# Performance work log

Hardware: AMD Instinct MI355X
Metric: run time of the kernel (lower is better)

Reference implementation:

```python
import jax, jax.numpy as jnp
from jax import lax
import numpy as np

N_NODES = 8192
N_FEATURES = 1024
N_FILTRATIONS = 4
HIDDEN_DIM = 64
MAX_DEG = 8            # fixed out-degree used when generating edge_list
N_EDGES = N_NODES * MAX_DEG


def setup_inputs() -> dict:
    key = jax.random.key(0)
    ks = jax.random.split(key, 10)
    X = jax.random.normal(ks[0], (N_NODES, N_FEATURES), dtype=jnp.float32)
    # directed edge list, exactly MAX_DEG out-edges per node
    src = jnp.repeat(jnp.arange(N_NODES, dtype=jnp.int32), MAX_DEG)
    dst = jax.random.randint(ks[1], (N_EDGES,), 0, N_NODES, dtype=jnp.int32)
    edge_list = jnp.stack([src, dst], axis=0)
    # filtrations_nn: Linear(n_features,32) -> ReLU -> Linear(32,n_filtrations)
    W1 = jax.random.normal(ks[2], (32, N_FEATURES), dtype=jnp.float32) * 0.05
    b1 = jnp.zeros((32,), jnp.float32)
    W2 = jax.random.normal(ks[3], (N_FILTRATIONS, 32), dtype=jnp.float32) * 0.05
    b2 = jnp.zeros((N_FILTRATIONS,), jnp.float32)
    # deep sets: theta = Linear(2*n_filtrations, hidden), rho = Linear(1, n_features)
    Wt = jax.random.normal(ks[4], (HIDDEN_DIM, 2 * N_FILTRATIONS), dtype=jnp.float32) * 0.05
    bt = jnp.zeros((HIDDEN_DIM,), jnp.float32)
    Wr = jax.random.normal(ks[5], (N_FEATURES, 1), dtype=jnp.float32) * 0.05
    br = jnp.zeros((N_FEATURES,), jnp.float32)
    return {"X": X, "edge_list": edge_list, "W1": W1, "b1": b1, "W2": W2,
            "b2": b2, "Wt": Wt, "bt": bt, "Wr": Wr, "br": br}


def uf_find(parent, node):
    # chase parent pointers until a root (parent[v] == v)
    return lax.while_loop(lambda v: parent[v] != v, lambda v: parent[v], node)


def build_neighbor_table(edge_list, n_nodes, max_deg):
    # padded CSR-style neighbor table (n_nodes, max_deg), -1 = no edge
    src = edge_list[0].astype(jnp.int32)
    dst = edge_list[1].astype(jnp.int32)
    e = src.shape[0]
    order_e = jnp.argsort(src)  # stable
    src_s, dst_s = src[order_e], dst[order_e]
    counts = jnp.zeros(n_nodes, jnp.int32).at[src].add(1)
    offsets = jnp.concatenate([jnp.zeros(1, jnp.int32), jnp.cumsum(counts)[:-1].astype(jnp.int32)])
    slot = jnp.arange(e, dtype=jnp.int32) - offsets[src_s]
    return jnp.full((n_nodes, max_deg), -1, jnp.int32).at[src_s, slot].set(dst_s)


def persistence_dim0(values, nbr_table):
    """0-dim persistence via sequential union-find with elder rule.
    Row for sort-position j: (birth=j, death=step when the component born at j is absorbed).
    Returned indexed by node id (diagram[order[j]] = row j), matching the torch code."""
    n = values.shape[0]
    order = jnp.argsort(values).astype(jnp.int32)  # filtration order
    pos = jnp.zeros(n, jnp.int32).at[order].set(jnp.arange(n, dtype=jnp.int32))  # rank
    parent0 = jnp.arange(n, dtype=jnp.int32)
    deaths0 = jnp.zeros(n, jnp.float32)

    def step_fn(carry, sv):
        parent, deaths = carry
        s, vertex = sv
        nbrs = nbr_table[vertex]

        def edge_body(k, pc):
            parent, deaths = pc
            u = nbrs[k]
            u_c = jnp.maximum(u, 0)
            valid = (u >= 0) & (pos[u_c] <= s)  # neighbor already activated
            u_eff = jnp.where(valid, u_c, vertex)
            r1 = uf_find(parent, vertex)
            r2 = uf_find(parent, u_eff)
            parent = parent.at[vertex].set(r1).at[u_eff].set(r2)  # path compression
            merge = r1 != r2
            older_is_r1 = pos[r1] < pos[r2]
            absorbed = jnp.where(older_is_r1, r2, r1)   # younger root dies (elder rule)
            survivor = jnp.where(older_is_r1, r1, r2)
            parent = parent.at[absorbed].set(jnp.where(merge, survivor, absorbed))
            dp = pos[absorbed]
            deaths = deaths.at[dp].set(jnp.where(merge, s.astype(jnp.float32), deaths[dp]))
            return (parent, deaths)

        parent, deaths = lax.fori_loop(0, MAX_DEG, edge_body, (parent, deaths))
        return (parent, deaths), None

    (_, deaths), _ = lax.scan(step_fn, (parent0, deaths0),
                              (jnp.arange(n, dtype=jnp.int32), order))
    # finalize: undying components -> inf in the original; use finite cap n for numerics
    deaths = jnp.where(deaths == 0.0, jnp.float32(n), deaths)
    births = jnp.arange(n, dtype=jnp.float32)
    diag_sorted = jnp.stack([births, deaths], axis=1)  # (n, 2), row j = sort position j
    return jnp.zeros((n, 2), jnp.float32).at[order].set(diag_sorted)


def reference(X, edge_list, W1, b1, W2, b2, Wt, bt, Wr, br):
    n = X.shape[0]
    # filtrations_nn
    h = jax.nn.relu(X @ W1.T + b1)
    filt = h @ W2.T + b2                      # (n, n_filtrations)
    filt_ng = lax.stop_gradient(filt)         # diagram is piecewise constant in filt
    nbr_table = build_neighbor_table(edge_list, n, MAX_DEG)
    pds = [persistence_dim0(filt_ng[:, i], nbr_table) for i in range(N_FILTRATIONS)]
    pd = jnp.stack(pds, axis=0).transpose(1, 0, 2).reshape(n, 2 * N_FILTRATIONS)
    # DeepSetsAggregation(theta, rho) with index=zeros(hidden_dim), dim=1:
    theta = pd @ Wt.T + bt                    # (n, hidden)
    pooled = jnp.sum(theta, axis=1, keepdims=True)  # segment-sum of dim 1 into one bucket
    x_hat = pooled @ Wr.T + br                # (n, n_features)
    return X + x_hat
```

## Files before the change

### kernel.cpp

```cpp
#include <hip/hip_runtime.h>

#define N_NODES     8192
#define N_FEAT      1024
#define N_FILT      4
#define MAXDEG      8
#define BLK         256

__global__ __launch_bounds__(256) void filt_kernel(
    const float* __restrict__ X, const float* __restrict__ W1,
    const float* __restrict__ b1, const float* __restrict__ W2,
    const float* __restrict__ b2, float* __restrict__ filtT)
{
    const int node = blockIdx.x * 8 + (threadIdx.x >> 5);
    const int h    = threadIdx.x & 31;
    const float* xr = X  + (size_t)node * N_FEAT;
    const float* wr = W1 + (size_t)h    * N_FEAT;
    float acc = 0.f;
    for (int j = 0; j < N_FEAT; j += 4) {
        float4 xv = *reinterpret_cast<const float4*>(xr + j);
        float4 wv = *reinterpret_cast<const float4*>(wr + j);
        acc += xv.x * wv.x + xv.y * wv.y + xv.z * wv.z + xv.w * wv.w;
    }
    float hv = fmaxf(acc + b1[h], 0.f);
    #pragma unroll
    for (int fo = 0; fo < N_FILT; ++fo) {
        float v = hv * W2[fo * 32 + h];
        for (int off = 16; off; off >>= 1) v += __shfl_xor(v, off, 32);
        if (h == 0) filtT[fo * N_NODES + node] = v + b2[fo];
    }
}

__global__ void wsum_kernel(const float* __restrict__ Wt,
                            const float* __restrict__ bt,
                            float* __restrict__ wsum)
{
    int t = threadIdx.x;
    if (t < 8) {
        float s = 0.f;
        for (int hh = 0; hh < 64; ++hh) s += Wt[hh * 8 + t];
        wsum[t] = s;
    } else if (t == 8) {
        float s = 0.f;
        for (int hh = 0; hh < 64; ++hh) s += bt[hh];
        wsum[8] = s;
    }
}

__global__ __launch_bounds__(256) void rank_partial_kernel(
    const float* __restrict__ filtT, unsigned short* __restrict__ partial)
{
    const int b  = blockIdx.x;
    const int f  = b >> 7;
    const int cs = (b >> 5) & 3;
    const int cv = b & 31;
    const int v  = (cv << 8) + threadIdx.x;
    const float myv = filtT[(f << 13) + v];

    __shared__ float4 tile[512];
    const float4* src = reinterpret_cast<const float4*>(filtT + (f << 13) + cs * 2048);
    for (int i = threadIdx.x; i < 512; i += 256) tile[i] = src[i];
    __syncthreads();

    int cnt = 0;
    const int ubase = cs * 2048;
    #pragma unroll 4
    for (int j = 0; j < 512; ++j) {
        float4 wv = tile[j];
        int u = ubase + j * 4;
        cnt += (wv.x < myv) || (wv.x == myv && (u + 0) < v);
        cnt += (wv.y < myv) || (wv.y == myv && (u + 1) < v);
        cnt += (wv.z < myv) || (wv.z == myv && (u + 2) < v);
        cnt += (wv.w < myv) || (wv.w == myv && (u + 3) < v);
    }
    partial[((f * 4 + cs) << 13) + v] = (unsigned short)cnt;
}

__global__ __launch_bounds__(256) void rank_final_kernel(
    const unsigned short* __restrict__ partial,
    unsigned short* __restrict__ pos16, unsigned short* __restrict__ order16)
{
    int g = blockIdx.x * 256 + threadIdx.x;
    int f = g >> 13, v = g & 8191;
    int r = (int)partial[((f * 4 + 0) << 13) + v]
          + (int)partial[((f * 4 + 1) << 13) + v]
          + (int)partial[((f * 4 + 2) << 13) + v]
          + (int)partial[((f * 4 + 3) << 13) + v];
    pos16[(f << 13) + v] = (unsigned short)r;
    order16[(f << 13) + r] = (unsigned short)v;
}

__global__ __launch_bounds__(256) void etable_kernel(
    const unsigned short* __restrict__ order16,
    const unsigned short* __restrict__ pos16,
    const int* __restrict__ edge_dst,
    unsigned short* __restrict__ et)
{
    const int f  = blockIdx.x >> 5;
    const int e0 = ((blockIdx.x & 31) << 11);
    for (int i = threadIdx.x; i < 2048; i += 256) {
        int e = e0 + i;
        int s = e >> 3, k = e & 7;
        int v = (int)order16[(f << 13) + s];
        int u = edge_dst[v * MAXDEG + k];
        int q = (int)pos16[(f << 13) + u];
        et[(size_t)f * (N_NODES * MAXDEG) + e] = (unsigned short)(q < s ? q : s);
    }
}

__device__ __forceinline__ int row8min(int v) {
    int t = min(v, __builtin_amdgcn_mov_dpp(v, 0xB1, 0xF, 0xF, true));
    t = min(t, __builtin_amdgcn_mov_dpp(t, 0x4E, 0xF, 0xF, true));
    t = min(t, __builtin_amdgcn_mov_dpp(t, 0x141, 0xF, 0xF, true));
    return t;
}

__global__ __launch_bounds__(256) void persist_kernel(
    const unsigned short* __restrict__ et,
    const unsigned short* __restrict__ pos16,
    unsigned short* __restrict__ death16)
{
    const int f    = blockIdx.x;
    const int tid  = threadIdx.x;
    const int lane = tid & 63;
    const int w    = tid >> 6;

    __shared__ unsigned int   s_pd[N_NODES];
    __shared__ unsigned short s_r16[BLK][8];
    __shared__ unsigned short s_list[BLK];
    __shared__ int s_wc[4];
    volatile unsigned int* vpd = s_pd;

    for (int v = tid; v < N_NODES; v += 256) s_pd[v] = (unsigned)v;
    __syncthreads();

    const unsigned short* etf = et + (size_t)f * (N_NODES * MAXDEG);

    for (int lo = 0; lo < N_NODES; lo += BLK) {
        const int s = lo + tid;

        uint4 raw = *reinterpret_cast<const uint4*>(etf + (size_t)s * 8);
        int e8[8];
        e8[0] = raw.x & 0xffff; e8[1] = raw.x >> 16;
        e8[2] = raw.y & 0xffff; e8[3] = raw.y >> 16;
        e8[4] = raw.z & 0xffff; e8[5] = raw.z >> 16;
        e8[6] = raw.w & 0xffff; e8[7] = raw.w >> 16;

        int pk[8];
        #pragma unroll
        for (int k = 0; k < 8; ++k) pk[k] = e8[k];
        for (;;) {
            int qk[8];
            #pragma unroll
            for (int k = 0; k < 8; ++k) qk[k] = (int)(vpd[pk[k]] & 0xffffu);
            bool done = true;
            #pragma unroll
            for (int k = 0; k < 8; ++k) { done &= (qk[k] == pk[k]); pk[k] = qk[k]; }
            if (done) break;
        }
        int first = -1; bool same = true;
        #pragma unroll
        for (int k = 0; k < 8; ++k) {
            if (e8[k] == s) continue;
            if (first < 0) first = pk[k];
            else same &= (pk[k] == first);
        }
        bool cand = (first >= 0) && !same;
        if (first >= 0 && same)
            vpd[s] = (unsigned)first | ((unsigned)s << 16);

        __syncthreads();

        bool impure = false;
        if (cand) {
            for (;;) {
                int qk[8];
                #pragma unroll
                for (int k = 0; k < 8; ++k) qk[k] = (int)(vpd[pk[k]] & 0xffffu);
                bool done = true;
                #pragma unroll
                for (int k = 0; k < 8; ++k) { done &= (qk[k] == pk[k]); pk[k] = qk[k]; }
                if (done) break;
            }
            int f2 = -1; bool same2 = true;
            #pragma unroll
            for (int k = 0; k < 8; ++k) {
                if (e8[k] == s) continue;
                if (f2 < 0) f2 = pk[k];
                else same2 &= (pk[k] == f2);
            }
            if (same2) {
                vpd[s] = (unsigned)f2 | ((unsigned)s << 16);
            } else {
                impure = true;
                #pragma unroll
                for (int k = 0; k < 8; ++k) s_r16[tid][k] = (unsigned short)pk[k];
            }
        }

        unsigned long long bal = __ballot(impure);
        int within = __popcll(bal & ((1ull << lane) - 1ull));
        if (lane == 0) s_wc[w] = __popcll(bal);
        __syncthreads();
        int base = 0, total = 0;
        #pragma unroll
        for (int i = 0; i < 4; ++i) { int c = s_wc[i]; if (i < w) base += c; total += c; }
        if (impure) s_list[base + within] = (unsigned short)tid;
        __syncthreads();

        if (tid < 64 && total > 0) {
            int t_cur = (int)s_list[0];
            int p_cur = (int)s_r16[t_cur][lane & 7];
            for (int i = 0; i < total; ++i) {
                int t_nxt = (int)s_list[(i + 1 < total) ? (i + 1) : i];
                int p_nxt = (int)s_r16[t_nxt][lane & 7];
                const int sv = lo + t_cur;
                int p = p_cur;
                for (;;) {
                    int q = (int)(vpd[p] & 0xffffu);
                    if (__all(q == p)) break;
                    p = q;
                }
                int m = row8min(p);
                if (lane < 8 && p != m)
                    vpd[p] = (unsigned)m | ((unsigned)sv << 16);
                if (lane == 0)
                    vpd[sv] = (unsigned)m | ((unsigned)sv << 16);
                t_cur = t_nxt; p_cur = p_nxt;
            }
        }
        __syncthreads();
    }

    for (int n = tid; n < N_NODES; n += 256) {
        int p = (int)pos16[(f << 13) + n];
        int d = (int)(s_pd[p] >> 16);
        death16[(f << 13) + n] = (unsigned short)(d ? d : N_NODES);
    }
}

__global__ __launch_bounds__(256) void out_kernel(
    const float* __restrict__ X, const float* __restrict__ Wr,
    const float* __restrict__ br,
    const unsigned short* __restrict__ pos16,
    const unsigned short* __restrict__ death16,
    const float* __restrict__ wsum,
    float* __restrict__ out)
{
    const int node = blockIdx.x;
    float pl = wsum[8];
    #pragma unroll
    for (int i = 0; i < N_FILT; ++i) {
        pl += (float)pos16[(i << 13) + node]   * wsum[2 * i + 0]
            + (float)death16[(i << 13) + node] * wsum[2 * i + 1];
    }
    const int fb = threadIdx.x * 4;
    const float4 xv = *reinterpret_cast<const float4*>(X + (size_t)node * N_FEAT + fb);
    const float4 wv = *reinterpret_cast<const float4*>(Wr + fb);
    const float4 bv = *reinterpret_cast<const float4*>(br + fb);
    float4 o;
    o.x = xv.x + pl * wv.x + bv.x;
    o.y = xv.y + pl * wv.y + bv.y;
    o.z = xv.z + pl * wv.z + bv.z;
    o.w = xv.w + pl * wv.w + bv.w;
    *reinterpret_cast<float4*>(out + (size_t)node * N_FEAT + fb) = o;
}

extern "C" void kernel_launch(void* const* d_in, const int* in_sizes, int n_in,
                              void* d_out, int out_size, void* d_ws, size_t ws_size,
                              hipStream_t stream) {
    const float* X  = (const float*)d_in[0];
    const int* edge = (const int*)d_in[1];
    const float* W1 = (const float*)d_in[2];
    const float* b1 = (const float*)d_in[3];
    const float* W2 = (const float*)d_in[4];
    const float* b2 = (const float*)d_in[5];
    const float* Wt = (const float*)d_in[6];
    const float* bt = (const float*)d_in[7];
    const float* Wr = (const float*)d_in[8];
    const float* br = (const float*)d_in[9];

    const int* edge_dst = edge + N_NODES * MAXDEG;

    char* wsb = (char*)d_ws;
    float*          filtT   = (float*)(wsb);
    unsigned short* pos16   = (unsigned short*)(wsb + 131072);
    unsigned short* order16 = (unsigned short*)(wsb + 196608);
    unsigned short* death16 = (unsigned short*)(wsb + 196608);
    unsigned short* partial = (unsigned short*)(wsb + 262144);
    unsigned short* et      = (unsigned short*)(wsb + 262144);
    float*          wsum    = (float*)(wsb + 786432);

    hipLaunchKernelGGL(filt_kernel,  dim3(N_NODES / 8), dim3(256), 0, stream,
                       X, W1, b1, W2, b2, filtT);
    hipLaunchKernelGGL(wsum_kernel,  dim3(1), dim3(64), 0, stream, Wt, bt, wsum);
    hipLaunchKernelGGL(rank_partial_kernel, dim3(512), dim3(256), 0, stream,
                       filtT, partial);
    hipLaunchKernelGGL(rank_final_kernel, dim3(128), dim3(256), 0, stream,
                       partial, pos16, order16);
    hipLaunchKernelGGL(etable_kernel, dim3(4 * 32), dim3(256), 0, stream,
                       order16, pos16, edge_dst, et);
    hipLaunchKernelGGL(persist_kernel, dim3(N_FILT), dim3(256), 0, stream,
                       et, pos16, death16);
    hipLaunchKernelGGL(out_kernel,   dim3(N_NODES), dim3(256), 0, stream,
                       X, Wr, br, pos16, death16, wsum, (float*)d_out);
}
```

Before: 640.3 us.

## Warp-specialize persistence loop to overlap impure-merge resolution with next block

The persistence kernel now splits each block into three producer warps and one consumer warp. The producers classify nodes of chunk `it` into double-buffered impure lists, while warp 0 runs the serial union-find merges for chunk `it-1`. This hides the serial resolution phase behind the parallel classification and drops one barrier per chunk. It risks producers reading partially updated union-find state and marking more nodes impure, and it leaves fewer lanes for classification. Separately, the tiny wsum kernel is removed and each out_kernel block recomputes the sums into shared memory, saving one launch at the cost of redundant small reads.

```diff
diff --git a/kernel.cpp b/kernel.cpp
--- a/kernel.cpp
+++ b/kernel.cpp
@@ -5,6 +5,7 @@
 #define N_FILT      4
 #define MAXDEG      8
 #define BLK         256
+#define NB          (N_NODES / BLK)
 
 __global__ __launch_bounds__(256) void filt_kernel(
     const float* __restrict__ X, const float* __restrict__ W1,
@@ -27,22 +28,6 @@
         float v = hv * W2[fo * 32 + h];
         for (int off = 16; off; off >>= 1) v += __shfl_xor(v, off, 32);
         if (h == 0) filtT[fo * N_NODES + node] = v + b2[fo];
-    }
-}
-
-__global__ void wsum_kernel(const float* __restrict__ Wt,
-                            const float* __restrict__ bt,
-                            float* __restrict__ wsum)
-{
-    int t = threadIdx.x;
-    if (t < 8) {
-        float s = 0.f;
-        for (int hh = 0; hh < 64; ++hh) s += Wt[hh * 8 + t];
-        wsum[t] = s;
-    } else if (t == 8) {
-        float s = 0.f;
-        for (int hh = 0; hh < 64; ++hh) s += bt[hh];
-        wsum[8] = s;
     }
 }
 
@@ -122,12 +107,11 @@
     const int f    = blockIdx.x;
     const int tid  = threadIdx.x;
     const int lane = tid & 63;
-    const int w    = tid >> 6;
 
     __shared__ unsigned int   s_pd[N_NODES];
-    __shared__ unsigned short s_r16[BLK][8];
-    __shared__ unsigned short s_list[BLK];
-    __shared__ int s_wc[4];
+    __shared__ unsigned short s_r16[2][BLK][8];
+    __shared__ unsigned short s_list[2][3 * 96];
+    __shared__ int s_wc[2][3];
     volatile unsigned int* vpd = s_pd;
 
     for (int v = tid; v < N_NODES; v += 256) s_pd[v] = (unsigned)v;
@@ -135,97 +119,111 @@
 
     const unsigned short* etf = et + (size_t)f * (N_NODES * MAXDEG);
 
-    for (int lo = 0; lo < N_NODES; lo += BLK) {
-        const int s = lo + tid;
-
-        uint4 raw = *reinterpret_cast<const uint4*>(etf + (size_t)s * 8);
-        int e8[8];
-        e8[0] = raw.x & 0xffff; e8[1] = raw.x >> 16;
-        e8[2] = raw.y & 0xffff; e8[3] = raw.y >> 16;
-        e8[4] = raw.z & 0xffff; e8[5] = raw.z >> 16;
-        e8[6] = raw.w & 0xffff; e8[7] = raw.w >> 16;
-
-        int pk[8];
-        #pragma unroll
-        for (int k = 0; k < 8; ++k) pk[k] = e8[k];
-        for (;;) {
-            int qk[8];
-            #pragma unroll
-            for (int k = 0; k < 8; ++k) qk[k] = (int)(vpd[pk[k]] & 0xffffu);
-            bool done = true;
-            #pragma unroll
-            for (int k = 0; k < 8; ++k) { done &= (qk[k] == pk[k]); pk[k] = qk[k]; }
-            if (done) break;
-        }
-        int first = -1; bool same = true;
-        #pragma unroll
-        for (int k = 0; k < 8; ++k) {
-            if (e8[k] == s) continue;
-            if (first < 0) first = pk[k];
-            else same &= (pk[k] == first);
-        }
-        bool cand = (first >= 0) && !same;
-        if (first >= 0 && same)
-            vpd[s] = (unsigned)first | ((unsigned)s << 16);
-
-        __syncthreads();
-
-        bool impure = false;
-        if (cand) {
-            for (;;) {
-                int qk[8];
+    for (int it = 0; it <= NB; ++it) {
+        if (tid >= 64) {
+            if (it < NB) {
+                const int lo  = it * BLK;
+                const int w   = (tid >> 6) - 1;
+                const int buf = it & 1;
+                const int cbase = (w == 0) ? 0 : (w == 1 ? 86 : 171);
+                const int csize = (w == 0) ? 86 : 85;
+                int nimp = 0;
                 #pragma unroll
-                for (int k = 0; k < 8; ++k) qk[k] = (int)(vpd[pk[k]] & 0xffffu);
-                bool done = true;
-                #pragma unroll
-                for (int k = 0; k < 8; ++k) { done &= (qk[k] == pk[k]); pk[k] = qk[k]; }
-                if (done) break;
+                for (int rnd = 0; rnd < 2; ++rnd) {
+                    const int off = rnd * 64 + lane;
+                    const bool active = (off < csize);
+                    const int sl = cbase + off;
+                    const int s  = lo + sl;
+                    bool impure = false;
+                    int pk[8];
+                    if (active) {
+                        uint4 raw = *reinterpret_cast<const uint4*>(etf + (size_t)s * 8);
+                        int e8[8];
+                        e8[0] = raw.x & 0xffff; e8[1] = raw.x >> 16;
+                        e8[2] = raw.y & 0xffff; e8[3] = raw.y >> 16;
+                        e8[4] = raw.z & 0xffff; e8[5] = raw.z >> 16;
+                        e8[6] = raw.w & 0xffff; e8[7] = raw.w >> 16;
+                        #pragma unroll
+                        for (int k = 0; k < 8; ++k) pk[k] = e8[k];
+                        for (;;) {
+                            int qk[8];
+                            #pragma unroll
+                            for (int k = 0; k < 8; ++k) qk[k] = (int)(vpd[pk[k]] & 0xffffu);
+                            bool done = true;
+                            #pragma unroll
+                            for (int k = 0; k < 8; ++k) { done &= (qk[k] == pk[k]); pk[k] = qk[k]; }
+                            if (done) break;
+                        }
+                        int first = -1; bool same = true;
+                        #pragma unroll
+                        for (int k = 0; k < 8; ++k) {
+                            if (e8[k] == s) continue;
+                            if (first < 0) first = pk[k];
+                            else same &= (pk[k] == first);
+                        }
+                        if (first >= 0 && same) {
+                            vpd[s] = (unsigned)first | ((unsigned)s << 16);
+                        } else if (first >= 0) {
+                            for (;;) {
+                                int qk[8];
+                                #pragma unroll
+                                for (int k = 0; k < 8; ++k) qk[k] = (int)(vpd[pk[k]] & 0xffffu);
+                                bool done = true;
+                                #pragma unroll
+                                for (int k = 0; k < 8; ++k) { done &= (qk[k] == pk[k]); pk[k] = qk[k]; }
+                                if (done) break;
+                            }
+                            int f2 = -1; bool same2 = true;
+                            #pragma unroll
+                            for (int k = 0; k < 8; ++k) {
+                                if (e8[k] == s) continue;
+                                if (f2 < 0) f2 = pk[k];
+                                else same2 &= (pk[k] == f2);
+                            }
+                            if (same2) vpd[s] = (unsigned)f2 | ((unsigned)s << 16);
+                            else impure = true;
+                        }
+                    }
+                    unsigned long long bal = __ballot(impure);
+                    int within = __popcll(bal & ((1ull << lane) - 1ull));
+                    if (impure) {
+                        s_list[buf][w * 96 + nimp + within] = (unsigned short)sl;
+                        #pragma unroll
+                        for (int k = 0; k < 8; ++k)
+                            s_r16[buf][sl][k] = (unsigned short)pk[k];
+                    }
+                    nimp += __popcll(bal);
+                }
+                if (lane == 0) s_wc[buf][w] = nimp;
             }
-            int f2 = -1; bool same2 = true;
-            #pragma unroll
-            for (int k = 0; k < 8; ++k) {
-                if (e8[k] == s) continue;
-                if (f2 < 0) f2 = pk[k];
-                else same2 &= (pk[k] == f2);
-            }
-            if (same2) {
-                vpd[s] = (unsigned)f2 | ((unsigned)s << 16);
-            } else {
-                impure = true;
-                #pragma unroll
-                for (int k = 0; k < 8; ++k) s_r16[tid][k] = (unsigned short)pk[k];
-            }
-        }
-
-        unsigned long long bal = __ballot(impure);
-        int within = __popcll(bal & ((1ull << lane) - 1ull));
-        if (lane == 0) s_wc[w] = __popcll(bal);
-        __syncthreads();
-        int base = 0, total = 0;
-        #pragma unroll
-        for (int i = 0; i < 4; ++i) { int c = s_wc[i]; if (i < w) base += c; total += c; }
-        if (impure) s_list[base + within] = (unsigned short)tid;
-        __syncthreads();
-
-        if (tid < 64 && total > 0) {
-            int t_cur = (int)s_list[0];
-            int p_cur = (int)s_r16[t_cur][lane & 7];
-            for (int i = 0; i < total; ++i) {
-                int t_nxt = (int)s_list[(i + 1 < total) ? (i + 1) : i];
-                int p_nxt = (int)s_r16[t_nxt][lane & 7];
-                const int sv = lo + t_cur;
-                int p = p_cur;
-                for (;;) {
-                    int q = (int)(vpd[p] & 0xffffu);
-                    if (__all(q == p)) break;
-                    p = q;
+        } else {
+            if (it > 0) {
+                const int lo  = (it - 1) * BLK;
+                const int buf = (it - 1) & 1;
+                for (int seg = 0; seg < 3; ++seg) {
+                    const int cnt = s_wc[buf][seg];
+                    if (cnt == 0) continue;
+                    const unsigned short* lst = &s_list[buf][seg * 96];
+                    int t_cur = (int)lst[0];
+                    int p_cur = (int)s_r16[buf][t_cur][lane & 7];
+                    for (int i = 0; i < cnt; ++i) {
+                        int t_nxt = (int)lst[(i + 1 < cnt) ? (i + 1) : i];
+                        int p_nxt = (int)s_r16[buf][t_nxt][lane & 7];
+                        const int sv = lo + t_cur;
+                        int p = p_cur;
+                        for (;;) {
+                            int q = (int)(vpd[p] & 0xffffu);
+                            if (__all(q == p)) break;
+                            p = q;
+                        }
+                        int m = row8min(p);
+                        if (lane < 8 && p != m)
+                            vpd[p] = (unsigned)m | ((unsigned)sv << 16);
+                        if (lane == 0)
+                            vpd[sv] = (unsigned)m | ((unsigned)sv << 16);
+                        t_cur = t_nxt; p_cur = p_nxt;
+                    }
                 }
-                int m = row8min(p);
-                if (lane < 8 && p != m)
-                    vpd[p] = (unsigned)m | ((unsigned)sv << 16);
-                if (lane == 0)
-                    vpd[sv] = (unsigned)m | ((unsigned)sv << 16);
-                t_cur = t_nxt; p_cur = p_nxt;
             }
         }
         __syncthreads();
@@ -243,15 +241,29 @@
     const float* __restrict__ br,
     const unsigned short* __restrict__ pos16,
     const unsigned short* __restrict__ death16,
-    const float* __restrict__ wsum,
+    const float* __restrict__ Wt, const float* __restrict__ bt,
     float* __restrict__ out)
 {
+    __shared__ float s_ws[9];
     const int node = blockIdx.x;
-    float pl = wsum[8];
+    if (threadIdx.x < 9) {
+        float s = 0.f;
+        if (threadIdx.x < 8) {
+            #pragma unroll 8
+            for (int hh = 0; hh < 64; ++hh) s += Wt[hh * 8 + threadIdx.x];
+        } else {
+            #pragma unroll 8
+            for (int hh = 0; hh < 64; ++hh) s += bt[hh];
+        }
+        s_ws[threadIdx.x] = s;
+    }
+    __syncthreads();
+
+    float pl = s_ws[8];
     #pragma unroll
     for (int i = 0; i < N_FILT; ++i) {
-        pl += (float)pos16[(i << 13) + node]   * wsum[2 * i + 0]
-            + (float)death16[(i << 13) + node] * wsum[2 * i + 1];
+        pl += (float)pos16[(i << 13) + node]   * s_ws[2 * i + 0]
+            + (float)death16[(i << 13) + node] * s_ws[2 * i + 1];
     }
     const int fb = threadIdx.x * 4;
     const float4 xv = *reinterpret_cast<const float4*>(X + (size_t)node * N_FEAT + fb);
@@ -288,11 +300,9 @@
     unsigned short* death16 = (unsigned short*)(wsb + 196608);
     unsigned short* partial = (unsigned short*)(wsb + 262144);
     unsigned short* et      = (unsigned short*)(wsb + 262144);
-    float*          wsum    = (float*)(wsb + 786432);
 
     hipLaunchKernelGGL(filt_kernel,  dim3(N_NODES / 8), dim3(256), 0, stream,
                        X, W1, b1, W2, b2, filtT);
-    hipLaunchKernelGGL(wsum_kernel,  dim3(1), dim3(64), 0, stream, Wt, bt, wsum);
     hipLaunchKernelGGL(rank_partial_kernel, dim3(512), dim3(256), 0, stream,
                        filtT, partial);
     hipLaunchKernelGGL(rank_final_kernel, dim3(128), dim3(256), 0, stream,
@@ -302,5 +312,5 @@
     hipLaunchKernelGGL(persist_kernel, dim3(N_FILT), dim3(256), 0, stream,
                        et, pos16, death16);
     hipLaunchKernelGGL(out_kernel,   dim3(N_NODES), dim3(256), 0, stream,
-                       X, Wr, br, pos16, death16, wsum, (float*)d_out);
-}
+                       X, Wr, br, pos16, death16, Wt, bt, (float*)d_out);
+}
```

After: 747.5 us. +16.8%, slower.

## Use idle waves to pre-compress pending root pointers during serial union phase

Applied to the files above, without the earlier changes.

While wave 0 serially processes the impure union list, the other three waves now spin and repeatedly advance the stored neighbor-root entries of the not-yet-processed items one pointer hop closer to their roots. Wave 0 publishes its progress and a completion token through volatile shared variables. The aim is to shorten the find chains on the serial critical path. The cost is shared-memory traffic and bank contention from the helper waves, plus fragile synchronization through volatile flags and a race on entries being overwritten while wave 0 reads them.

```diff
diff --git a/kernel.cpp b/kernel.cpp
--- a/kernel.cpp
+++ b/kernel.cpp
@@ -128,15 +128,23 @@
     __shared__ unsigned short s_r16[BLK][8];
     __shared__ unsigned short s_list[BLK];
     __shared__ int s_wc[4];
-    volatile unsigned int* vpd = s_pd;
+    __shared__ int s_tok;
+    __shared__ int s_prog;
+    volatile unsigned int*   vpd  = s_pd;
+    volatile unsigned short* vr16 = &s_r16[0][0];
+    volatile int* vtok  = &s_tok;
+    volatile int* vprog = &s_prog;
 
     for (int v = tid; v < N_NODES; v += 256) s_pd[v] = (unsigned)v;
+    if (tid == 0) { s_tok = 0; s_prog = 0; }
     __syncthreads();
 
     const unsigned short* etf = et + (size_t)f * (N_NODES * MAXDEG);
-
-    for (int lo = 0; lo < N_NODES; lo += BLK) {
-        const int s = lo + tid;
+    const int NB = N_NODES / BLK;
+
+    for (int it = 0; it < NB; ++it) {
+        const int lo = it * BLK;
+        const int s  = lo + tid;
 
         uint4 raw = *reinterpret_cast<const uint4*>(etf + (size_t)s * 8);
         int e8[8];
@@ -167,6 +175,7 @@
         bool cand = (first >= 0) && !same;
         if (first >= 0 && same)
             vpd[s] = (unsigned)first | ((unsigned)s << 16);
+        if (tid == 0) *vprog = 0;
 
         __syncthreads();
 
@@ -207,25 +216,43 @@
         if (impure) s_list[base + within] = (unsigned short)tid;
         __syncthreads();
 
-        if (tid < 64 && total > 0) {
-            int t_cur = (int)s_list[0];
-            int p_cur = (int)s_r16[t_cur][lane & 7];
-            for (int i = 0; i < total; ++i) {
-                int t_nxt = (int)s_list[(i + 1 < total) ? (i + 1) : i];
-                int p_nxt = (int)s_r16[t_nxt][lane & 7];
-                const int sv = lo + t_cur;
-                int p = p_cur;
-                for (;;) {
-                    int q = (int)(vpd[p] & 0xffffu);
-                    if (__all(q == p)) break;
-                    p = q;
+        if (tid < 64) {
+            if (total > 0) {
+                int t_cur = (int)s_list[0];
+                int p_cur = (int)vr16[t_cur * 8 + (lane & 7)];
+                for (int i = 0; i < total; ++i) {
+                    if (lane == 0) *vprog = i;
+                    int t_nxt = (int)s_list[(i + 1 < total) ? (i + 1) : i];
+                    int p_nxt = (int)vr16[t_nxt * 8 + (lane & 7)];
+                    const int sv = lo + t_cur;
+                    int p = p_cur;
+                    for (;;) {
+                        int q = (int)(vpd[p] & 0xffffu);
+                        if (__all(q == p)) break;
+                        p = q;
+                    }
+                    int m = row8min(p);
+                    if (lane < 8 && p != m)
+                        vpd[p] = (unsigned)m | ((unsigned)sv << 16);
+                    if (lane == 0)
+                        vpd[sv] = (unsigned)m | ((unsigned)sv << 16);
+                    t_cur = t_nxt; p_cur = p_nxt;
                 }
-                int m = row8min(p);
-                if (lane < 8 && p != m)
-                    vpd[p] = (unsigned)m | ((unsigned)sv << 16);
-                if (lane == 0)
-                    vpd[sv] = (unsigned)m | ((unsigned)sv << 16);
-                t_cur = t_nxt; p_cur = p_nxt;
+            }
+            if (lane == 0) *vtok = it + 1;
+        } else {
+            const int hw = w - 1;
+            const int il = lane >> 3;
+            const int sl = lane & 7;
+            while (*vtok < it + 1) {
+                int start = *vprog;
+                for (int i = start + hw * 8 + il; i < total; i += 24) {
+                    int t = (int)s_list[i];
+                    int r = (int)vr16[t * 8 + sl];
+                    int q = (int)(vpd[r] & 0xffffu);
+                    if (q != r) vr16[t * 8 + sl] = (unsigned short)q;
+                }
+                __builtin_amdgcn_s_sleep(1);
             }
         }
         __syncthreads();
```

After: 671.5 us. 4.9% more time.

## Software-pipeline persistence union-find: overlap serial merges with next block's chasing

Applied to the files above, without the earlier changes.

Restructures the per-filtration union-find loop into a two-stage pipeline with double-buffered shared state. Wave 0 performs the serial impure-merge pass for the previous block while waves 1-3 chase roots for the current block, and the current node's parent is set to the min root early. This hides the single-wave serial merge latency behind parallel work and drops one barrier per block. The catch is that three waves now cover 256 slots with two passes, and reading parents while they are being merged concurrently relies on the chase being tolerant of stale links.

```diff
diff --git a/kernel.cpp b/kernel.cpp
--- a/kernel.cpp
+++ b/kernel.cpp
@@ -5,6 +5,7 @@
 #define N_FILT      4
 #define MAXDEG      8
 #define BLK         256
+#define NB          (N_NODES / BLK)
 
 __global__ __launch_bounds__(256) void filt_kernel(
     const float* __restrict__ X, const float* __restrict__ W1,
@@ -114,6 +115,18 @@
     return t;
 }
 
+__device__ __forceinline__ void chase8(volatile unsigned int* vpd, int (&pk)[8]) {
+    for (;;) {
+        int qk[8];
+        #pragma unroll
+        for (int k = 0; k < 8; ++k) qk[k] = (int)(vpd[pk[k]] & 0xffffu);
+        bool done = true;
+        #pragma unroll
+        for (int k = 0; k < 8; ++k) { done &= (qk[k] == pk[k]); pk[k] = qk[k]; }
+        if (done) break;
+    }
+}
+
 __global__ __launch_bounds__(256) void persist_kernel(
     const unsigned short* __restrict__ et,
     const unsigned short* __restrict__ pos16,
@@ -125,9 +138,10 @@
     const int w    = tid >> 6;
 
     __shared__ unsigned int   s_pd[N_NODES];
-    __shared__ unsigned short s_r16[BLK][8];
-    __shared__ unsigned short s_list[BLK];
-    __shared__ int s_wc[4];
+    __shared__ unsigned short s_r16[2][BLK][8];
+    __shared__ unsigned char  s_flag[2][BLK];
+    __shared__ unsigned short s_list[2][BLK];
+    __shared__ int s_wc[2][4];
     volatile unsigned int* vpd = s_pd;
 
     for (int v = tid; v < N_NODES; v += 256) s_pd[v] = (unsigned)v;
@@ -135,98 +149,114 @@
 
     const unsigned short* etf = et + (size_t)f * (N_NODES * MAXDEG);
 
-    for (int lo = 0; lo < N_NODES; lo += BLK) {
-        const int s = lo + tid;
-
-        uint4 raw = *reinterpret_cast<const uint4*>(etf + (size_t)s * 8);
-        int e8[8];
-        e8[0] = raw.x & 0xffff; e8[1] = raw.x >> 16;
-        e8[2] = raw.y & 0xffff; e8[3] = raw.y >> 16;
-        e8[4] = raw.z & 0xffff; e8[5] = raw.z >> 16;
-        e8[6] = raw.w & 0xffff; e8[7] = raw.w >> 16;
-
-        int pk[8];
-        #pragma unroll
-        for (int k = 0; k < 8; ++k) pk[k] = e8[k];
-        for (;;) {
-            int qk[8];
+    for (int it = 0; it <= NB; ++it) {
+        const int buf = it & 1;
+
+        if (w == 0) {
+            if (it > 0) {
+                const int pbuf = (it - 1) & 1;
+                const int plo  = (it - 1) * BLK;
+                const int total = s_wc[pbuf][0] + s_wc[pbuf][1]
+                                + s_wc[pbuf][2] + s_wc[pbuf][3];
+                if (total > 0) {
+                    int t_cur = (int)s_list[pbuf][0];
+                    int p_cur = (int)s_r16[pbuf][t_cur][lane & 7];
+                    for (int i = 0; i < total; ++i) {
+                        int nidx  = (i + 1 < total) ? (i + 1) : i;
+                        int t_nxt = (int)s_list[pbuf][nidx];
+                        int p_nxt = (int)s_r16[pbuf][t_nxt][lane & 7];
+                        const int sv = plo + t_cur;
+                        int p = p_cur;
+                        for (;;) {
+                            int q = (int)(vpd[p] & 0xffffu);
+                            if (__all(q == p)) break;
+                            p = q;
+                        }
+                        int m = row8min(p);
+                        if (lane < 8 && p != m)
+                            vpd[p] = (unsigned)m | ((unsigned)sv << 16);
+                        t_cur = t_nxt; p_cur = p_nxt;
+                    }
+                }
+            }
+        } else if (it < NB) {
+            const int lo = it * BLK;
+            const int h  = tid - 64;
             #pragma unroll
-            for (int k = 0; k < 8; ++k) qk[k] = (int)(vpd[pk[k]] & 0xffffu);
-            bool done = true;
-            #pragma unroll
-            for (int k = 0; k < 8; ++k) { done &= (qk[k] == pk[k]); pk[k] = qk[k]; }
-            if (done) break;
-        }
-        int first = -1; bool same = true;
-        #pragma unroll
-        for (int k = 0; k < 8; ++k) {
-            if (e8[k] == s) continue;
-            if (first < 0) first = pk[k];
-            else same &= (pk[k] == first);
-        }
-        bool cand = (first >= 0) && !same;
-        if (first >= 0 && same)
-            vpd[s] = (unsigned)first | ((unsigned)s << 16);
-
-        __syncthreads();
-
-        bool impure = false;
-        if (cand) {
-            for (;;) {
-                int qk[8];
+            for (int rep = 0; rep < 2; ++rep) {
+                const int sl = (rep == 0) ? h : (192 + h);
+                if (rep == 1 && h >= 64) break;
+                const int s = lo + sl;
+                uint4 raw = *reinterpret_cast<const uint4*>(etf + (size_t)s * 8);
+                int e8[8];
+                e8[0] = raw.x & 0xffff; e8[1] = raw.x >> 16;
+                e8[2] = raw.y & 0xffff; e8[3] = raw.y >> 16;
+                e8[4] = raw.z & 0xffff; e8[5] = raw.z >> 16;
+                e8[6] = raw.w & 0xffff; e8[7] = raw.w >> 16;
+                int pk[8];
                 #pragma unroll
-                for (int k = 0; k < 8; ++k) qk[k] = (int)(vpd[pk[k]] & 0xffffu);
-                bool done = true;
+                for (int k = 0; k < 8; ++k) pk[k] = e8[k];
+                chase8(vpd, pk);
+                int first = -1; bool same = true;
                 #pragma unroll
-                for (int k = 0; k < 8; ++k) { done &= (qk[k] == pk[k]); pk[k] = qk[k]; }
-                if (done) break;
-            }
-            int f2 = -1; bool same2 = true;
-            #pragma unroll
-            for (int k = 0; k < 8; ++k) {
-                if (e8[k] == s) continue;
-                if (f2 < 0) f2 = pk[k];
-                else same2 &= (pk[k] == f2);
-            }
-            if (same2) {
-                vpd[s] = (unsigned)f2 | ((unsigned)s << 16);
-            } else {
-                impure = true;
-                #pragma unroll
-                for (int k = 0; k < 8; ++k) s_r16[tid][k] = (unsigned short)pk[k];
+                for (int k = 0; k < 8; ++k) {
+                    if (e8[k] == s) continue;
+                    if (first < 0) first = pk[k];
+                    else same &= (pk[k] == first);
+                }
+                if (first < 0) {
+                    s_flag[buf][sl] = 0;
+                } else if (same) {
+                    vpd[s] = (unsigned)first | ((unsigned)s << 16);
+                    s_flag[buf][sl] = 0;
+                } else {
+                    s_flag[buf][sl] = 2;
+                    #pragma unroll
+                    for (int k = 0; k < 8; ++k)
+                        s_r16[buf][sl][k] = (unsigned short)pk[k];
+                }
             }
         }
-
+        __syncthreads();
+
+        bool impure = false;
+        int  within = 0;
+        if (it < NB) {
+            const int sl = tid;
+            const int s  = it * BLK + sl;
+            if (s_flag[buf][sl] == 2) {
+                int pk[8];
+                #pragma unroll
+                for (int k = 0; k < 8; ++k) pk[k] = (int)s_r16[buf][sl][k];
+                chase8(vpd, pk);
+                int first = -1; bool same = true; int m = pk[0];
+                #pragma unroll
+                for (int k = 0; k < 8; ++k) {
+                    m = min(m, pk[k]);
+                    if (pk[k] == s) continue;
+                    if (first < 0) first = pk[k];
+                    else same &= (pk[k] == first);
+                }
+                if (same) {
+                    vpd[s] = (unsigned)first | ((unsigned)s << 16);
+                } else {
+                    impure = true;
+                    #pragma unroll
+                    for (int k = 0; k < 8; ++k)
+                        s_r16[buf][sl][k] = (unsigned short)pk[k];
+                    vpd[s] = (unsigned)m | ((unsigned)s << 16);
+                }
+            }
+        }
         unsigned long long bal = __ballot(impure);
-        int within = __popcll(bal & ((1ull << lane) - 1ull));
-        if (lane == 0) s_wc[w] = __popcll(bal);
+        within = __popcll(bal & ((1ull << lane) - 1ull));
+        if (it < NB && lane == 0) s_wc[buf][w] = __popcll(bal);
         __syncthreads();
-        int base = 0, total = 0;
-        #pragma unroll
-        for (int i = 0; i < 4; ++i) { int c = s_wc[i]; if (i < w) base += c; total += c; }
-        if (impure) s_list[base + within] = (unsigned short)tid;
-        __syncthreads();
-
-        if (tid < 64 && total > 0) {
-            int t_cur = (int)s_list[0];
-            int p_cur = (int)s_r16[t_cur][lane & 7];
-            for (int i = 0; i < total; ++i) {
-                int t_nxt = (int)s_list[(i + 1 < total) ? (i + 1) : i];
-                int p_nxt = (int)s_r16[t_nxt][lane & 7];
-                const int sv = lo + t_cur;
-                int p = p_cur;
-                for (;;) {
-                    int q = (int)(vpd[p] & 0xffffu);
-                    if (__all(q == p)) break;
-                    p = q;
-                }
-                int m = row8min(p);
-                if (lane < 8 && p != m)
-                    vpd[p] = (unsigned)m | ((unsigned)sv << 16);
-                if (lane == 0)
-                    vpd[sv] = (unsigned)m | ((unsigned)sv << 16);
-                t_cur = t_nxt; p_cur = p_nxt;
-            }
+        if (it < NB && impure) {
+            int base = 0;
+            #pragma unroll
+            for (int i = 0; i < 4; ++i) { if (i < w) base += s_wc[buf][i]; }
+            s_list[buf][base + within] = (unsigned short)tid;
         }
         __syncthreads();
     }
```

New measurement: 646.3 us. Within noise of the previous version (+0.9%).
